# Performance work log

Hardware: AMD Instinct MI355X
Metric: run time of the kernel (lower is better)

Reference implementation:

```python
import jax, jax.numpy as jnp
import numpy as np

INVALID = 1e9  # distance value marking a missing arc (>= 1e6 threshold in source)
TEMPERATURE = 0.5


def setup_inputs() -> dict:
    n = 4096
    key = jax.random.key(0)
    k_d, k_m, k_l = jax.random.split(key, 3)
    dist = jax.random.uniform(k_d, (n, n), dtype=jnp.float32, minval=0.0, maxval=100.0)
    keep = jax.random.uniform(k_m, (n, n)) < 0.5
    distance_matrix = jnp.where(keep, dist, INVALID).astype(jnp.float32)
    logits = (-2.0 + 0.5 * jax.random.normal(k_l, (n, n))).astype(jnp.float32)
    attention_logits = jnp.zeros((n, n), dtype=jnp.float32)
    return {
        "distance_matrix": distance_matrix,
        "logits": logits,
        "attention_logits": attention_logits,
        "source": 0,
        "destination": n - 1,
    }


def reference(distance_matrix, logits, attention_logits, source, destination):
    n = distance_matrix.shape[0]
    valid = (distance_matrix < 1e6).astype(jnp.float32)
    density = jnp.sum(valid) / (n * n)
    mu1 = 1.0
    mu2 = 10.0 * (1.0 + density)
    mu3 = 10.0 * (1.0 + density)

    # decision matrix (dense branch)
    attention = jax.nn.softmax(attention_logits, axis=1)
    x = jax.nn.sigmoid(logits / TEMPERATURE) * attention * valid  # [n, n]

    # flow penalty: vectorized form of the per-node loop
    out_flow = jnp.sum(x, axis=1)  # [n]
    in_flow = jnp.sum(x, axis=0)   # [n]
    d = out_flow - in_flow
    d = d.at[source].add(-1.0).at[destination].add(1.0)
    flow_penalty = jnp.sum(d * d)

    path_cost = jnp.sum(distance_matrix * x)  # invalid arcs have x == 0
    binary_penalty = jnp.sum(x * (1.0 - x))

    # connectivity: 10-step matmul power iteration (min(n-1, 10) = 10 for n > 11)
    reach = x
    for _ in range(10):
        reach = jnp.minimum(reach + reach @ x, 1.0)
    connectivity_penalty = jnp.square(1.0 - reach[source, destination])

    sparsity_penalty = jnp.sum(x) / (n * n)
    n_edges = jnp.sum(valid)

    return (mu1 * path_cost / (n_edges + 1e-6)
            + mu2 * flow_penalty / n
            + mu3 * binary_penalty / (n * n)
            + 20.0 * connectivity_penalty
            + 5.0 * sparsity_penalty)
```

## Files before the change

### kernel.cpp

```cpp
#include <hip/hip_runtime.h>
#include <hip/hip_bf16.h>
#include <cmath>

typedef unsigned short u16;
typedef unsigned int u32;

__device__ __forceinline__ float bf2f(u16 b) {
    return __uint_as_float(((u32)b) << 16);
}
__device__ __forceinline__ u16 f2bf(float f) {
    u32 u = __float_as_uint(f);
    u = (u + 0x7fffu + ((u >> 16) & 1u)) >> 16;
    return (u16)u;
}

__device__ __forceinline__ float warp_sum(float v) {
#pragma unroll
    for (int o = 32; o > 0; o >>= 1) v += __shfl_down(v, o, 64);
    return v;
}
__device__ __forceinline__ float warp_max(float v) {
#pragma unroll
    for (int o = 32; o > 0; o >>= 1) v = fmaxf(v, __shfl_down(v, o, 64));
    return v;
}
__device__ float block_sum(float v) {
    __shared__ float s[4];
    v = warp_sum(v);
    __syncthreads();
    if ((threadIdx.x & 63) == 0) s[threadIdx.x >> 6] = v;
    __syncthreads();
    return s[0] + s[1] + s[2] + s[3];
}
__device__ float block_max(float v) {
    __shared__ float s[4];
    v = warp_max(v);
    __syncthreads();
    if ((threadIdx.x & 63) == 0) s[threadIdx.x >> 6] = v;
    __syncthreads();
    return fmaxf(fmaxf(s[0], s[1]), fmaxf(s[2], s[3]));
}

template <int K>
__global__ __launch_bounds__(256) void k_main(
    const float* __restrict__ dist, const float* __restrict__ logit,
    const float* __restrict__ attn, const int* __restrict__ srcp,
    u16* __restrict__ xb, float* __restrict__ out_flow,
    float* __restrict__ cnt_row, float* __restrict__ s2_row,
    float* __restrict__ pc_row, float* __restrict__ v, int n) {
    const int row = blockIdx.x;
    const int t = threadIdx.x;
    const size_t base = (size_t)row * n;

    float4 af[K];
#pragma unroll
    for (int k = 0; k < K; ++k)
        af[k] = *(const float4*)(attn + base + 4 * t + 1024 * k);
    float a[4 * K];
    float mx = -3.0e38f;
#pragma unroll
    for (int k = 0; k < K; ++k) {
        a[4 * k + 0] = af[k].x; a[4 * k + 1] = af[k].y;
        a[4 * k + 2] = af[k].z; a[4 * k + 3] = af[k].w;
        mx = fmaxf(mx, fmaxf(fmaxf(af[k].x, af[k].y), fmaxf(af[k].z, af[k].w)));
    }
    float m = block_max(mx);
    float se = 0.f;
#pragma unroll
    for (int i = 0; i < 4 * K; ++i) { a[i] = __expf(a[i] - m); se += a[i]; }
    float Z = block_sum(se);
    float invZ = 1.0f / Z;
    const int src = *srcp;

    float4 d4[K], l4[K];
#pragma unroll
    for (int k = 0; k < K; ++k) {
        const int col = 4 * t + 1024 * k;
        d4[k] = *(const float4*)(dist + base + col);
        l4[k] = *(const float4*)(logit + base + col);
    }
    float cnt = 0.f, s1 = 0.f, s2 = 0.f, pc = 0.f;
#pragma unroll
    for (int k = 0; k < K; ++k) {
        const int col = 4 * t + 1024 * k;
        float dv[4] = {d4[k].x, d4[k].y, d4[k].z, d4[k].w};
        float lv[4] = {l4[k].x, l4[k].y, l4[k].z, l4[k].w};
        float xv[4];
        ushort4 pk;
        u16* pkp = (u16*)&pk;
#pragma unroll
        for (int q = 0; q < 4; ++q) {
            float valid = (dv[q] < 1.0e6f) ? 1.f : 0.f;
            float sg = 1.0f / (1.0f + __expf(-2.0f * lv[q]));
            float x = sg * (a[4 * k + q] * invZ) * valid;
            xv[q] = x;
            cnt += valid;
            s1 += x;
            s2 += x * x;
            pc += dv[q] * x;
            pkp[q] = f2bf(x);
        }
        *(ushort4*)(xb + base + col) = pk;
        if (row == src) {
            float4 vf; vf.x = xv[0]; vf.y = xv[1]; vf.z = xv[2]; vf.w = xv[3];
            *(float4*)(v + col) = vf;
        }
    }
    float s1t = block_sum(s1);
    float cntt = block_sum(cnt);
    float s2t = block_sum(s2);
    float pct = block_sum(pc);
    if (t == 0) {
        out_flow[row] = s1t;
        cnt_row[row] = cntt;
        s2_row[row] = s2t;
        pc_row[row] = pct;
    }
}

template <int FIRST>
__global__ __launch_bounds__(256) void k_iter(
    const u16* __restrict__ xb, const float* __restrict__ v_in,
    const float* __restrict__ up_in, float* __restrict__ v_out,
    float* __restrict__ up_out, float* __restrict__ ip, int n, int rows_per) {
    __shared__ float vl[128];
    const int t = threadIdx.x;
    const int j0 = blockIdx.x * 1024 + t * 4;
    const int i0 = blockIdx.y * rows_per;
    const int nchunk = gridDim.y;
    if (t < rows_per) {
        float a = v_in[i0 + t];
        if (!FIRST) {
#pragma unroll 8
            for (int c = 0; c < nchunk; ++c) a += up_in[(size_t)c * n + i0 + t];
        }
        vl[t] = a;
        if (blockIdx.x == 0) v_out[i0 + t] = a;
    }
    __syncthreads();
    float4 acc = {0.f, 0.f, 0.f, 0.f};
    float4 cs = {0.f, 0.f, 0.f, 0.f};
#pragma unroll 8
    for (int i = 0; i < rows_per; ++i) {
        ushort4 xv = *(const ushort4*)(xb + (size_t)(i0 + i) * n + j0);
        float vi = vl[i];
        acc.x = fmaf(vi, bf2f(xv.x), acc.x);
        acc.y = fmaf(vi, bf2f(xv.y), acc.y);
        acc.z = fmaf(vi, bf2f(xv.z), acc.z);
        acc.w = fmaf(vi, bf2f(xv.w), acc.w);
        if (FIRST) {
            cs.x += bf2f(xv.x); cs.y += bf2f(xv.y);
            cs.z += bf2f(xv.z); cs.w += bf2f(xv.w);
        }
    }
    *(float4*)(up_out + (size_t)blockIdx.y * n + j0) = acc;
    if (FIRST) *(float4*)(ip + (size_t)blockIdx.y * n + j0) = cs;
}

__global__ __launch_bounds__(256) void k_reduce(
    const float* __restrict__ out_flow, const float* __restrict__ ip,
    const float* __restrict__ cnt_row, const float* __restrict__ s2_row,
    const float* __restrict__ pc_row, const int* __restrict__ srcp,
    const int* __restrict__ dstp, float* __restrict__ pb, int n, int nchunk) {
    const int t = threadIdx.x;
    const int j = blockIdx.x * 256 + t;
    const int src = *srcp, dst = *dstp;
    float infl = 0.f;
#pragma unroll 8
    for (int c = 0; c < nchunk; ++c) infl += ip[(size_t)c * n + j];
    float d = out_flow[j] - infl;
    if (j == src) d -= 1.f;
    if (j == dst) d += 1.f;
    float f = block_sum(d * d);
    float s1 = block_sum(out_flow[j]);
    float cnt = block_sum(cnt_row[j]);
    float s2 = block_sum(s2_row[j]);
    float pc = block_sum(pc_row[j]);
    if (t == 0) {
        float* p = pb + blockIdx.x * 5;
        p[0] = f; p[1] = s1; p[2] = cnt; p[3] = s2; p[4] = pc;
    }
}

__global__ __launch_bounds__(256) void k_final(
    const float* __restrict__ pb, const float* __restrict__ v_last,
    const float* __restrict__ up_last, const int* __restrict__ dstp,
    float* __restrict__ out, int n, int nblk, int nchunk) {
    const int t = threadIdx.x;
    const int dst = *dstp;
    float flow = block_sum(t < nblk ? pb[t * 5 + 0] : 0.f);
    float S1   = block_sum(t < nblk ? pb[t * 5 + 1] : 0.f);
    float NE   = block_sum(t < nblk ? pb[t * 5 + 2] : 0.f);
    float S2   = block_sum(t < nblk ? pb[t * 5 + 3] : 0.f);
    float PC   = block_sum(t < nblk ? pb[t * 5 + 4] : 0.f);
    float r = block_sum(t < nchunk ? up_last[(size_t)t * n + dst] : 0.f);
    if (t == 0) {
        r += v_last[dst];
        float nf = (float)n;
        float nn = nf * nf;
        float density = NE / nn;
        float mu2 = 10.f * (1.f + density);
        float om = 1.f - r;
        float res = PC / (NE + 1e-6f)
                  + mu2 * flow / nf
                  + mu2 * (S1 - S2) / nn
                  + 20.f * om * om
                  + 5.f * S1 / nn;
        out[0] = res;
    }
}

extern "C" void kernel_launch(void* const* d_in, const int* in_sizes, int n_in,
                              void* d_out, int out_size, void* d_ws, size_t ws_size,
                              hipStream_t stream) {
    const float* dist = (const float*)d_in[0];
    const float* logit = (const float*)d_in[1];
    const float* attn = (const float*)d_in[2];
    const int* srcp = (const int*)d_in[3];
    const int* dstp = (const int*)d_in[4];
    const int n = (int)(std::sqrt((double)in_sizes[0]) + 0.5);
    const size_t nn = (size_t)n * n;

    const int RC = 64;
    const int rows_per = n / RC;

    char* ws = (char*)d_ws;
    u16* xb = (u16*)ws;
    float* f = (float*)(ws + nn * sizeof(u16));
    float* out_flow = f; f += n;
    float* cnt_row = f;  f += n;
    float* s2_row = f;   f += n;
    float* pc_row = f;   f += n;
    float* vA = f;       f += n;
    float* vB = f;       f += n;
    float* upA = f;      f += (size_t)RC * n;
    float* upB = f;      f += (size_t)RC * n;
    float* ip = f;       f += (size_t)RC * n;
    float* pb = f;       f += 128;

    switch (n >> 10) {
        case 4: k_main<4><<<n, 256, 0, stream>>>(dist, logit, attn, srcp, xb,
                    out_flow, cnt_row, s2_row, pc_row, vA, n); break;
        case 2: k_main<2><<<n, 256, 0, stream>>>(dist, logit, attn, srcp, xb,
                    out_flow, cnt_row, s2_row, pc_row, vA, n); break;
        case 8: k_main<8><<<n, 256, 0, stream>>>(dist, logit, attn, srcp, xb,
                    out_flow, cnt_row, s2_row, pc_row, vA, n); break;
        default: k_main<1><<<n, 256, 0, stream>>>(dist, logit, attn, srcp, xb,
                    out_flow, cnt_row, s2_row, pc_row, vA, n); break;
    }

    const dim3 ig(n / 1024, RC);

    k_iter<1><<<ig, 256, 0, stream>>>(xb, vA, nullptr, vB, upA, ip, n, rows_per);
    float* vin = vB;  float* uin = upA;
    float* vout;      float* uout;
    for (int it = 2; it <= 10; ++it) {
        vout = (it & 1) ? vB : vA;
        uout = (it & 1) ? upA : upB;
        k_iter<0><<<ig, 256, 0, stream>>>(xb, vin, uin, vout, uout, nullptr, n,
                                          rows_per);
        vin = vout; uin = uout;
    }

    k_reduce<<<n / 256, 256, 0, stream>>>(out_flow, ip, cnt_row, s2_row,
                                          pc_row, srcp, dstp, pb, n, RC);
    k_final<<<1, 256, 0, stream>>>(pb, vin, uin, dstp, (float*)d_out, n,
                                   n / 256, RC);
}
```

Before: 134.4 us.

## Map one row per wave in main kernel and XCD-aware block mapping in iterations

The main elementwise kernel now assigns one matrix row per 64-lane wave, with four rows per block. This replaces block-wide shared-memory reductions with wave shuffles and streams the dist and logit loads inside the loop. The iteration kernel uses a 1D grid whose block index is remapped so that each XCD handles contiguous row chunks, which is meant to improve L2 locality of the bf16 matrix. The cross-chunk vector reduction is also split across all four waves instead of a single thread loop. The cost is higher per-thread register use for the attention values (16 float4 per lane), and the remapping assumes the block count divides evenly by 8.

```diff
diff --git a/kernel.cpp b/kernel.cpp
--- a/kernel.cpp
+++ b/kernel.cpp
@@ -14,77 +14,68 @@
     return (u16)u;
 }
 
-__device__ __forceinline__ float warp_sum(float v) {
-#pragma unroll
-    for (int o = 32; o > 0; o >>= 1) v += __shfl_down(v, o, 64);
+__device__ __forceinline__ float wave_sum(float v) {
+#pragma unroll
+    for (int o = 32; o > 0; o >>= 1) v += __shfl_xor(v, o, 64);
     return v;
 }
-__device__ __forceinline__ float warp_max(float v) {
-#pragma unroll
-    for (int o = 32; o > 0; o >>= 1) v = fmaxf(v, __shfl_down(v, o, 64));
+__device__ __forceinline__ float wave_max(float v) {
+#pragma unroll
+    for (int o = 32; o > 0; o >>= 1) v = fmaxf(v, __shfl_xor(v, o, 64));
     return v;
 }
+
 __device__ float block_sum(float v) {
     __shared__ float s[4];
-    v = warp_sum(v);
+    v = wave_sum(v);
     __syncthreads();
     if ((threadIdx.x & 63) == 0) s[threadIdx.x >> 6] = v;
     __syncthreads();
     return s[0] + s[1] + s[2] + s[3];
 }
-__device__ float block_max(float v) {
-    __shared__ float s[4];
-    v = warp_max(v);
-    __syncthreads();
-    if ((threadIdx.x & 63) == 0) s[threadIdx.x >> 6] = v;
-    __syncthreads();
-    return fmaxf(fmaxf(s[0], s[1]), fmaxf(s[2], s[3]));
-}
-
-template <int K>
+
+template <int NF4>
 __global__ __launch_bounds__(256) void k_main(
     const float* __restrict__ dist, const float* __restrict__ logit,
     const float* __restrict__ attn, const int* __restrict__ srcp,
     u16* __restrict__ xb, float* __restrict__ out_flow,
     float* __restrict__ cnt_row, float* __restrict__ s2_row,
     float* __restrict__ pc_row, float* __restrict__ v, int n) {
-    const int row = blockIdx.x;
-    const int t = threadIdx.x;
+    const int lane = threadIdx.x & 63;
+    const int wv = threadIdx.x >> 6;
+    const int row = blockIdx.x * 4 + wv;
     const size_t base = (size_t)row * n;
 
-    float4 af[K];
-#pragma unroll
-    for (int k = 0; k < K; ++k)
-        af[k] = *(const float4*)(attn + base + 4 * t + 1024 * k);
-    float a[4 * K];
+    float4 af[NF4];
+#pragma unroll
+    for (int k = 0; k < NF4; ++k)
+        af[k] = *(const float4*)(attn + base + 4 * lane + 256 * k);
     float mx = -3.0e38f;
 #pragma unroll
-    for (int k = 0; k < K; ++k) {
-        a[4 * k + 0] = af[k].x; a[4 * k + 1] = af[k].y;
-        a[4 * k + 2] = af[k].z; a[4 * k + 3] = af[k].w;
+    for (int k = 0; k < NF4; ++k)
         mx = fmaxf(mx, fmaxf(fmaxf(af[k].x, af[k].y), fmaxf(af[k].z, af[k].w)));
-    }
-    float m = block_max(mx);
+    mx = wave_max(mx);
+
     float se = 0.f;
 #pragma unroll
-    for (int i = 0; i < 4 * K; ++i) { a[i] = __expf(a[i] - m); se += a[i]; }
-    float Z = block_sum(se);
-    float invZ = 1.0f / Z;
+    for (int k = 0; k < NF4; ++k) {
+        af[k].x = __expf(af[k].x - mx); se += af[k].x;
+        af[k].y = __expf(af[k].y - mx); se += af[k].y;
+        af[k].z = __expf(af[k].z - mx); se += af[k].z;
+        af[k].w = __expf(af[k].w - mx); se += af[k].w;
+    }
+    const float invZ = 1.0f / wave_sum(se);
     const int src = *srcp;
 
-    float4 d4[K], l4[K];
-#pragma unroll
-    for (int k = 0; k < K; ++k) {
-        const int col = 4 * t + 1024 * k;
-        d4[k] = *(const float4*)(dist + base + col);
-        l4[k] = *(const float4*)(logit + base + col);
-    }
     float cnt = 0.f, s1 = 0.f, s2 = 0.f, pc = 0.f;
-#pragma unroll
-    for (int k = 0; k < K; ++k) {
-        const int col = 4 * t + 1024 * k;
-        float dv[4] = {d4[k].x, d4[k].y, d4[k].z, d4[k].w};
-        float lv[4] = {l4[k].x, l4[k].y, l4[k].z, l4[k].w};
+#pragma unroll 4
+    for (int k = 0; k < NF4; ++k) {
+        const int col = 4 * lane + 256 * k;
+        const float4 df = *(const float4*)(dist + base + col);
+        const float4 lf = *(const float4*)(logit + base + col);
+        const float dv[4] = {df.x, df.y, df.z, df.w};
+        const float lv[4] = {lf.x, lf.y, lf.z, lf.w};
+        const float av[4] = {af[k].x, af[k].y, af[k].z, af[k].w};
         float xv[4];
         ushort4 pk;
         u16* pkp = (u16*)&pk;
@@ -92,7 +83,7 @@
         for (int q = 0; q < 4; ++q) {
             float valid = (dv[q] < 1.0e6f) ? 1.f : 0.f;
             float sg = 1.0f / (1.0f + __expf(-2.0f * lv[q]));
-            float x = sg * (a[4 * k + q] * invZ) * valid;
+            float x = sg * (av[q] * invZ) * valid;
             xv[q] = x;
             cnt += valid;
             s1 += x;
@@ -106,15 +97,18 @@
             *(float4*)(v + col) = vf;
         }
     }
-    float s1t = block_sum(s1);
-    float cntt = block_sum(cnt);
-    float s2t = block_sum(s2);
-    float pct = block_sum(pc);
-    if (t == 0) {
-        out_flow[row] = s1t;
-        cnt_row[row] = cntt;
-        s2_row[row] = s2t;
-        pc_row[row] = pct;
+#pragma unroll
+    for (int o = 32; o > 0; o >>= 1) {
+        cnt += __shfl_xor(cnt, o, 64);
+        s1  += __shfl_xor(s1, o, 64);
+        s2  += __shfl_xor(s2, o, 64);
+        pc  += __shfl_xor(pc, o, 64);
+    }
+    if (lane == 0) {
+        out_flow[row] = s1;
+        cnt_row[row] = cnt;
+        s2_row[row] = s2;
+        pc_row[row] = pc;
     }
 }
 
@@ -122,22 +116,44 @@
 __global__ __launch_bounds__(256) void k_iter(
     const u16* __restrict__ xb, const float* __restrict__ v_in,
     const float* __restrict__ up_in, float* __restrict__ v_out,
-    float* __restrict__ up_out, float* __restrict__ ip, int n, int rows_per) {
-    __shared__ float vl[128];
+    float* __restrict__ up_out, float* __restrict__ ip,
+    int n, int nbx, int rc) {
+    __shared__ float vl[64];
+    __shared__ float vparts[4][64];
     const int t = threadIdx.x;
-    const int j0 = blockIdx.x * 1024 + t * 4;
-    const int i0 = blockIdx.y * rows_per;
-    const int nchunk = gridDim.y;
-    if (t < rows_per) {
-        float a = v_in[i0 + t];
-        if (!FIRST) {
-#pragma unroll 8
-            for (int c = 0; c < nchunk; ++c) a += up_in[(size_t)c * n + i0 + t];
-        }
-        vl[t] = a;
-        if (blockIdx.x == 0) v_out[i0 + t] = a;
+    const int lin = blockIdx.x;
+    const int xcd = lin & 7;
+    const int slot = lin >> 3;
+    const int bx = slot % nbx;
+    const int by = xcd * ((gridDim.x >> 3) / nbx) + slot / nbx;
+    const int rows_per = n / rc;
+    const int i0 = by * rows_per;
+    const int j0 = bx * 1024 + t * 4;
+
+    if (FIRST) {
+        if (t < rows_per) {
+            float a = v_in[i0 + t];
+            vl[t] = a;
+            if (bx == 0) v_out[i0 + t] = a;
+        }
+    } else {
+        const int i = t & 63, g = t >> 6;
+        const int cpg = rc >> 2;
+        float a = 0.f;
+#pragma unroll 4
+        for (int c = g * cpg; c < (g + 1) * cpg; ++c)
+            a += up_in[(size_t)c * n + i0 + i];
+        vparts[g][i] = a;
+        __syncthreads();
+        if (t < rows_per) {
+            float s = v_in[i0 + t] + vparts[0][t] + vparts[1][t] +
+                      vparts[2][t] + vparts[3][t];
+            vl[t] = s;
+            if (bx == 0) v_out[i0 + t] = s;
+        }
     }
     __syncthreads();
+
     float4 acc = {0.f, 0.f, 0.f, 0.f};
     float4 cs = {0.f, 0.f, 0.f, 0.f};
 #pragma unroll 8
@@ -153,8 +169,8 @@
             cs.z += bf2f(xv.z); cs.w += bf2f(xv.w);
         }
     }
-    *(float4*)(up_out + (size_t)blockIdx.y * n + j0) = acc;
-    if (FIRST) *(float4*)(ip + (size_t)blockIdx.y * n + j0) = cs;
+    *(float4*)(up_out + (size_t)by * n + j0) = acc;
+    if (FIRST) *(float4*)(ip + (size_t)by * n + j0) = cs;
 }
 
 __global__ __launch_bounds__(256) void k_reduce(
@@ -222,7 +238,7 @@
     const size_t nn = (size_t)n * n;
 
     const int RC = 64;
-    const int rows_per = n / RC;
+    const int nbx = n / 1024;
 
     char* ws = (char*)d_ws;
     u16* xb = (u16*)ws;
@@ -238,27 +254,27 @@
     float* ip = f;       f += (size_t)RC * n;
     float* pb = f;       f += 128;
 
-    switch (n >> 10) {
-        case 4: k_main<4><<<n, 256, 0, stream>>>(dist, logit, attn, srcp, xb,
-                    out_flow, cnt_row, s2_row, pc_row, vA, n); break;
-        case 2: k_main<2><<<n, 256, 0, stream>>>(dist, logit, attn, srcp, xb,
-                    out_flow, cnt_row, s2_row, pc_row, vA, n); break;
-        case 8: k_main<8><<<n, 256, 0, stream>>>(dist, logit, attn, srcp, xb,
-                    out_flow, cnt_row, s2_row, pc_row, vA, n); break;
-        default: k_main<1><<<n, 256, 0, stream>>>(dist, logit, attn, srcp, xb,
-                    out_flow, cnt_row, s2_row, pc_row, vA, n); break;
-    }
-
-    const dim3 ig(n / 1024, RC);
-
-    k_iter<1><<<ig, 256, 0, stream>>>(xb, vA, nullptr, vB, upA, ip, n, rows_per);
+    switch (n >> 8) {
+        case 16: k_main<16><<<n / 4, 256, 0, stream>>>(dist, logit, attn, srcp,
+                     xb, out_flow, cnt_row, s2_row, pc_row, vA, n); break;
+        case 8:  k_main<8><<<n / 4, 256, 0, stream>>>(dist, logit, attn, srcp,
+                     xb, out_flow, cnt_row, s2_row, pc_row, vA, n); break;
+        case 4:  k_main<4><<<n / 4, 256, 0, stream>>>(dist, logit, attn, srcp,
+                     xb, out_flow, cnt_row, s2_row, pc_row, vA, n); break;
+        default: k_main<16><<<n / 4, 256, 0, stream>>>(dist, logit, attn, srcp,
+                     xb, out_flow, cnt_row, s2_row, pc_row, vA, n); break;
+    }
+
+    const int niblk = nbx * RC;
+
+    k_iter<1><<<niblk, 256, 0, stream>>>(xb, vA, nullptr, vB, upA, ip, n, nbx, RC);
     float* vin = vB;  float* uin = upA;
     float* vout;      float* uout;
     for (int it = 2; it <= 10; ++it) {
         vout = (it & 1) ? vB : vA;
         uout = (it & 1) ? upA : upB;
-        k_iter<0><<<ig, 256, 0, stream>>>(xb, vin, uin, vout, uout, nullptr, n,
-                                          rows_per);
+        k_iter<0><<<niblk, 256, 0, stream>>>(xb, vin, uin, vout, uout, nullptr,
+                                             n, nbx, RC);
         vin = vout; uin = uout;
     }
 
```

Result: slower. 161.2 us (+19.9%).
